# Kernel tuning notes

Measured on AMD Instinct MI355X. Metric: run time of the kernel, lower is better.

The kernel has to match this reference:

```python
import jax, jax.numpy as jnp
import numpy as np

HIDDEN = 4096
N_HEADS = 32
N_KV_HEADS = 8
HEAD_DIM = HIDDEN // N_HEADS
ROPE_BASE = 10000.0


def rotate_half(x):
    x1, x2 = jnp.split(x, 2, axis=-1)
    return jnp.concatenate((-x2, x1), axis=-1)


def rope_cos_sin(seq_len, dtype=jnp.float32):
    inv_freq = 1.0 / (ROPE_BASE ** (jnp.arange(0, HEAD_DIM, 2, dtype=jnp.float32) / HEAD_DIM))
    t = jnp.arange(seq_len, dtype=jnp.float32)
    freqs = jnp.einsum('i,j->ij', t, inv_freq)          # [S, D/2]
    emb = jnp.concatenate((freqs, freqs), axis=-1)       # [S, D]
    return jnp.cos(emb).astype(dtype), jnp.sin(emb).astype(dtype)


def setup_inputs() -> dict:
    key = jax.random.key(0)
    ks = jax.random.split(key, 6)
    bsz, q_len = 2, 2048
    hidden_states = jax.random.normal(ks[0], (bsz, q_len, HIDDEN), dtype=jnp.float32)
    # causal additive mask [bsz, 1, q, kv]
    neg = jnp.finfo(jnp.float32).min
    causal = jnp.where(jnp.tril(jnp.ones((q_len, q_len), dtype=bool)), 0.0, neg)
    attention_mask = jnp.broadcast_to(causal, (bsz, 1, q_len, q_len)).astype(jnp.float32)
    position_ids = jnp.broadcast_to(jnp.arange(q_len, dtype=jnp.int64), (bsz, q_len))
    s = 1.0 / np.sqrt(HIDDEN)
    Wq = jax.random.normal(ks[1], (HIDDEN, N_HEADS * HEAD_DIM), dtype=jnp.float32) * s
    Wk = jax.random.normal(ks[2], (HIDDEN, N_KV_HEADS * HEAD_DIM), dtype=jnp.float32) * s
    Wv = jax.random.normal(ks[3], (HIDDEN, N_KV_HEADS * HEAD_DIM), dtype=jnp.float32) * s
    Wo = jax.random.normal(ks[4], (N_HEADS * HEAD_DIM, HIDDEN), dtype=jnp.float32) * s
    return {"hidden_states": hidden_states, "attention_mask": attention_mask,
            "position_ids": position_ids, "Wq": Wq, "Wk": Wk, "Wv": Wv, "Wo": Wo}


def reference(hidden_states, attention_mask, position_ids, Wq, Wk, Wv, Wo):
    bsz, q_len, _ = hidden_states.shape
    groups = N_HEADS // N_KV_HEADS
    q = (hidden_states @ Wq).reshape(bsz, q_len, N_HEADS, HEAD_DIM).transpose(0, 2, 1, 3)
    k = (hidden_states @ Wk).reshape(bsz, q_len, N_KV_HEADS, HEAD_DIM).transpose(0, 2, 1, 3)
    v = (hidden_states @ Wv).reshape(bsz, q_len, N_KV_HEADS, HEAD_DIM).transpose(0, 2, 1, 3)
    cos, sin = rope_cos_sin(q_len, hidden_states.dtype)
    cos = cos[position_ids][:, None]  # [B,1,S,D]
    sin = sin[position_ids][:, None]
    q = q * cos + rotate_half(q) * sin
    k = k * cos + rotate_half(k) * sin
    # GQA: repeat_interleave KV heads
    k = jnp.repeat(k, groups, axis=1)
    v = jnp.repeat(v, groups, axis=1)
    scores = jnp.einsum('bhqd,bhkd->bhqk', q, k) / np.sqrt(HEAD_DIM)
    scores = scores + attention_mask
    attn = jax.nn.softmax(scores.astype(jnp.float32), axis=-1).astype(q.dtype)
    out = jnp.einsum('bhqk,bhkd->bhqd', attn, v)
    out = out.transpose(0, 2, 1, 3).reshape(bsz, q_len, HIDDEN)
    return out @ Wo
```

## Files before the change

kernel.cpp:

```cpp
#include <hip/hip_runtime.h>
#include <cstdint>
#include <type_traits>

typedef unsigned short u16;
typedef __attribute__((ext_vector_type(8))) short bf16x8;
typedef __attribute__((ext_vector_type(4))) float f32x4;

__device__ __forceinline__ u16 f2bf(float f) {
  unsigned u = __float_as_uint(f);
  u += 0x7fffu + ((u >> 16) & 1u);
  return (u16)(u >> 16);
}
__device__ __forceinline__ float bf2f(u16 h) {
  return __uint_as_float(((unsigned)h) << 16);
}
__device__ __forceinline__ unsigned cvtpk(float lo, float hi) {
  unsigned r;
  asm("v_cvt_pk_bf16_f32 %0, %1, %2" : "=v"(r) : "v"(lo), "v"(hi));
  return r;
}

__device__ __forceinline__ void glds16(const u16* g, u16* l) {
  __builtin_amdgcn_global_load_lds((const __attribute__((address_space(1))) void*)g,
                                   (__attribute__((address_space(3))) void*)l,
                                   16, 0, 0);
}

#define MFMA16(a, b, c) __builtin_amdgcn_mfma_f32_16x16x32_bf16((a), (b), (c), 0, 0, 0)

__global__ __launch_bounds__(256) void k_f32_to_bf16(const float* __restrict__ in,
                                                     u16* __restrict__ out, int n4) {
  int i = blockIdx.x * 256 + threadIdx.x;
  if (i < n4) {
    float4 v = ((const float4*)in)[i];
    ushort4 o;
    o.x = f2bf(v.x); o.y = f2bf(v.y); o.z = f2bf(v.z); o.w = f2bf(v.w);
    ((ushort4*)out)[i] = o;
  }
}

__global__ __launch_bounds__(256) void k_transpose_f32_bf16(const float* __restrict__ in,
                                                            u16* __restrict__ out,
                                                            int R, int C) {
  __shared__ float t[32][33];
  int tx = threadIdx.x & 31, ty = threadIdx.x >> 5;
  int c0 = blockIdx.x * 32, r0 = blockIdx.y * 32;
#pragma unroll
  for (int i = 0; i < 4; ++i)
    t[ty + 8 * i][tx] = in[(size_t)(r0 + ty + 8 * i) * C + c0 + tx];
  __syncthreads();
#pragma unroll
  for (int i = 0; i < 4; ++i)
    out[(size_t)(c0 + ty + 8 * i) * R + r0 + tx] = f2bf(t[tx][ty + 8 * i]);
}

template <typename OutT>
__global__ __launch_bounds__(512, 2) void k_gemm256(const u16* __restrict__ A,
                                                    const u16* __restrict__ B,
                                                    OutT* __restrict__ C,
                                                    int M, int N, int K) {
  __shared__ __align__(16) u16 lds[65536];
  const int tid = threadIdx.x, wave = tid >> 6, lane = tid & 63;
  const int quad = lane >> 4, l15 = lane & 15, l7 = l15 & 7;
  const int wr = wave >> 2, wc = wave & 3;

  const int nwg = gridDim.x * gridDim.y;
  const int bid = blockIdx.y * gridDim.x + blockIdx.x;
  const int swz = (bid & 7) * (nwg >> 3) + (bid >> 3);
  const int m0 = (swz / gridDim.x) * 256, n0 = (swz % gridDim.x) * 256;

  const int lrow = lane >> 3, lx = (lane & 7) ^ lrow;
  const size_t rowK = (size_t)K;
  const u16* Abase = A + (size_t)(m0 + wr * 128 + (wave & 3) * 8 + lrow) * rowK + lx * 8;
  const u16* Bbase = B + (size_t)(n0 + wave * 16 + lrow) * rowK + lx * 8;

  u16* const AT0 = lds;
  u16* const BT0 = lds + 16384;
  u16* const AT1 = lds + 32768;
  u16* const BT1 = lds + 49152;
  const int adst = (wr * 128 + (wave & 3) * 8) * 64;
  const int bdst = wave * 16 * 64;

#define STAGE_A(DST, la, kk) \
  glds16(Abase + (size_t)((la) * 32) * rowK + (kk), (DST) + adst + (la) * 2048)
#define STAGE_B(DST, g, kk)                                                      \
  glds16(Bbase + (size_t)((((g) >> 1) * 128 + ((g) & 1) * 8)) * rowK + (kk),     \
         (DST) + bdst + (((g) >> 1) * 128 + ((g) & 1) * 8) * 64)

  const int aoff = (wr * 128 + l15) * 64;
  const int boff = (wc * 64 + l15) * 64;
  const int ck0 = (quad ^ l7) * 8;
  const int ck1 = ((quad + 4) ^ l7) * 8;

  STAGE_B(BT0, 0, 0); STAGE_B(BT0, 1, 0); STAGE_B(BT0, 2, 0); STAGE_B(BT0, 3, 0);
  STAGE_A(AT0, 0, 0); STAGE_A(AT0, 1, 0); STAGE_A(AT0, 2, 0); STAGE_A(AT0, 3, 0);
  f32x4 acc[8][4] = {};
  asm volatile("s_waitcnt vmcnt(3)\ns_barrier" ::: "memory");

#define GPHASE(MP, STG1, STG2, VN)                                              \
  {                                                                             \
    bf16x8 a00 = *(const bf16x8*)&AT[aoff + (2 * (MP)) * 1024 + ck0];           \
    bf16x8 a01 = *(const bf16x8*)&AT[aoff + (2 * (MP)) * 1024 + ck1];           \
    bf16x8 a10 = *(const bf16x8*)&AT[aoff + (2 * (MP) + 1) * 1024 + ck0];       \
    bf16x8 a11 = *(const bf16x8*)&AT[aoff + (2 * (MP) + 1) * 1024 + ck1];       \
    STG1;                                                                       \
    STG2;                                                                       \
    asm volatile("s_barrier" ::: "memory");                                     \
    asm volatile("s_waitcnt lgkmcnt(0)" ::: "memory");                          \
    __builtin_amdgcn_sched_barrier(0);                                          \
    __builtin_amdgcn_s_setprio(1);                                              \
    _Pragma("unroll")                                                           \
    for (int nf = 0; nf < 4; ++nf) {                                            \
      acc[2 * (MP)][nf] = MFMA16(a00, bq[nf][0], acc[2 * (MP)][nf]);            \
      acc[2 * (MP)][nf] = MFMA16(a01, bq[nf][1], acc[2 * (MP)][nf]);            \
      acc[2 * (MP) + 1][nf] = MFMA16(a10, bq[nf][0], acc[2 * (MP) + 1][nf]);    \
      acc[2 * (MP) + 1][nf] = MFMA16(a11, bq[nf][1], acc[2 * (MP) + 1][nf]);    \
    }                                                                           \
    __builtin_amdgcn_s_setprio(0);                                              \
    asm volatile("s_waitcnt vmcnt(" #VN ")\ns_barrier" ::: "memory");           \
  }

  const int nt = K >> 6;
  for (int kt = 0; kt < nt; ++kt) {
    u16* const AT = (kt & 1) ? AT1 : AT0;
    u16* const BT = (kt & 1) ? BT1 : BT0;
    u16* const ATn = (kt & 1) ? AT0 : AT1;
    u16* const BTn = (kt & 1) ? BT0 : BT1;
    const int kk = (kt + 1 < nt) ? ((kt + 1) << 6) : 0;

    bf16x8 bq[4][2];
    {
      bf16x8 a00 = *(const bf16x8*)&AT[aoff + 0 * 1024 + ck0];
      bf16x8 a01 = *(const bf16x8*)&AT[aoff + 0 * 1024 + ck1];
      bf16x8 a10 = *(const bf16x8*)&AT[aoff + 1 * 1024 + ck0];
      bf16x8 a11 = *(const bf16x8*)&AT[aoff + 1 * 1024 + ck1];
#pragma unroll
      for (int nf = 0; nf < 4; ++nf) {
        bq[nf][0] = *(const bf16x8*)&BT[boff + nf * 1024 + ck0];
        bq[nf][1] = *(const bf16x8*)&BT[boff + nf * 1024 + ck1];
      }
      STAGE_B(BTn, 0, kk);
      STAGE_B(BTn, 1, kk);
      asm volatile("s_barrier" ::: "memory");
      asm volatile("s_waitcnt lgkmcnt(0)" ::: "memory");
      __builtin_amdgcn_sched_barrier(0);
      __builtin_amdgcn_s_setprio(1);
#pragma unroll
      for (int nf = 0; nf < 4; ++nf) {
        acc[0][nf] = MFMA16(a00, bq[nf][0], acc[0][nf]);
        acc[0][nf] = MFMA16(a01, bq[nf][1], acc[0][nf]);
        acc[1][nf] = MFMA16(a10, bq[nf][0], acc[1][nf]);
        acc[1][nf] = MFMA16(a11, bq[nf][1], acc[1][nf]);
      }
      __builtin_amdgcn_s_setprio(0);
      asm volatile("s_waitcnt vmcnt(4)\ns_barrier" ::: "memory");
    }
    GPHASE(1, STAGE_B(BTn, 2, kk), STAGE_B(BTn, 3, kk), 5)
    GPHASE(2, STAGE_A(ATn, 0, kk), STAGE_A(ATn, 1, kk), 6)
    GPHASE(3, STAGE_A(ATn, 2, kk), STAGE_A(ATn, 3, kk), 3)
  }
#undef GPHASE
#undef STAGE_A
#undef STAGE_B

  asm volatile("s_waitcnt vmcnt(0)" ::: "memory");

#pragma unroll
  for (int mf = 0; mf < 8; ++mf)
#pragma unroll
    for (int nf = 0; nf < 4; ++nf) {
      const int row = m0 + wr * 128 + mf * 16 + quad * 4;
      const int col = n0 + wc * 64 + nf * 16 + l15;
#pragma unroll
      for (int r = 0; r < 4; ++r) {
        float v = acc[mf][nf][r];
        if constexpr (std::is_same<OutT, u16>::value)
          C[(size_t)(row + r) * N + col] = f2bf(v);
        else
          C[(size_t)(row + r) * N + col] = v;
      }
    }
}

__global__ __launch_bounds__(256) void k_rope(u16* __restrict__ qkv) {
  int row = blockIdx.x;
  int s = row & 2047;
  u16* base = qkv + (size_t)row * 6144;
  for (int p = threadIdx.x; p < 2560; p += 256) {
    int d, col;
    if (p < 2048) { d = p & 63; col = (p >> 6) * 128 + d; }
    else { int pk = p - 2048; d = pk & 63; col = 4096 + (pk >> 6) * 128 + d; }
    float f = exp2f((float)d * (-13.287712379549449f / 64.0f));
    float th = (float)s * f;
    float c = cosf(th), sn = sinf(th);
    float x1 = bf2f(base[col]), x2 = bf2f(base[col + 64]);
    base[col]      = f2bf(x1 * c - x2 * sn);
    base[col + 64] = f2bf(x2 * c + x1 * sn);
  }
}

__global__ __launch_bounds__(256) void k_vt(const u16* __restrict__ qkv, u16* __restrict__ vt) {
  __shared__ u16 t[32][33];
  int tx = threadIdx.x & 31, ty = threadIdx.x >> 5;
  int s0 = blockIdx.x * 32, d0 = blockIdx.y * 32, g = blockIdx.z;
  int b = g >> 3, kvh = g & 7;
  const u16* in = qkv + (size_t)(b * 2048) * 6144 + 5120 + kvh * 128;
  u16* out = vt + (size_t)g * 128 * 2048;
#pragma unroll
  for (int i = 0; i < 4; ++i)
    t[ty + 8 * i][tx] = in[(size_t)(s0 + ty + 8 * i) * 6144 + d0 + tx];
  __syncthreads();
#pragma unroll
  for (int i = 0; i < 4; ++i)
    out[(size_t)(d0 + ty + 8 * i) * 2048 + s0 + tx] = t[tx][ty + 8 * i];
}

__global__ __launch_bounds__(256) void k_flash(const u16* __restrict__ qkv,
                                               const u16* __restrict__ vt,
                                               u16* __restrict__ ao) {
  __shared__ __align__(16) u16 Ks[64][128];
  __shared__ __align__(16) u16 Vs[128][64];
  __shared__ __align__(16) u16 Ps[4][16][64];
  const int tid = threadIdx.x, wave = tid >> 6, lane = tid & 63;
  const int quad = lane >> 4, l15 = lane & 15, l7 = l15 & 7;
  const int bh = blockIdx.x, b = bh >> 5, h = bh & 31, kvh = h >> 2;
  const int q0 = (31 - (int)blockIdx.y) * 64;

  bf16x8 aq[4];
  {
    const u16* qp = qkv + (size_t)(b * 2048 + q0 + wave * 16 + l15) * 6144 + h * 128 + quad * 8;
#pragma unroll
    for (int c = 0; c < 4; ++c) aq[c] = *(const bf16x8*)(qp + c * 32);
  }

  f32x4 oacc[8] = {};
  float m_r = -1e30f, l_r = 0.f;

  const u16* kbase = qkv + (size_t)(b * 2048) * 6144 + 4096 + kvh * 128;
  const u16* vbase = vt + (size_t)(b * 8 + kvh) * 128 * 2048;

  const int krow = wave * 4 + (lane >> 4);
  const int kch = (lane & 15) ^ (krow & 7);
  const u16* ksrc0 = kbase + (size_t)krow * 6144 + kch * 8;
  const int vrow = wave * 8 + (lane >> 3);
  const int vch = (lane & 7) ^ (vrow & 7);
  const u16* vsrc0 = vbase + (size_t)vrow * 2048 + vch * 8;
  u16* KsW = &Ks[0][0] + wave * 512;
  u16* VsW = &Vs[0][0] + wave * 512;

  const float SC = 0.12751744f;
  const int qg = q0 + wave * 16 + l15;
  const int nk = q0 / 64 + 1;

  for (int kt = 0; kt < nk; ++kt) {
    const int k0 = kt * 64;
    __syncthreads();
#pragma unroll
    for (int it = 0; it < 4; ++it)
      glds16(ksrc0 + (size_t)(k0 + it * 16) * 6144, KsW + it * 2048);
#pragma unroll
    for (int it = 0; it < 4; ++it)
      glds16(vsrc0 + k0 + it * 65536, VsW + it * 2048);
    __syncthreads();

    f32x4 sacc[4] = {};
    __builtin_amdgcn_s_setprio(1);
#pragma unroll
    for (int c = 0; c < 4; ++c)
#pragma unroll
      for (int nt = 0; nt < 4; ++nt) {
        const bf16x8 bk = *(const bf16x8*)&Ks[nt * 16 + l15][((4 * c + quad) ^ l7) * 8];
        sacc[nt] = __builtin_amdgcn_mfma_f32_16x16x32_bf16(bk, aq[c], sacc[nt], 0, 0, 0);
      }
    __builtin_amdgcn_s_setprio(0);

    float p[16];
    if (kt == nk - 1) {
#pragma unroll
      for (int nt = 0; nt < 4; ++nt)
#pragma unroll
        for (int r = 0; r < 4; ++r) {
          const float v = sacc[nt][r] * SC;
          p[nt * 4 + r] = (k0 + nt * 16 + quad * 4 + r > qg) ? -3e38f : v;
        }
    } else {
#pragma unroll
      for (int nt = 0; nt < 4; ++nt)
#pragma unroll
        for (int r = 0; r < 4; ++r) p[nt * 4 + r] = sacc[nt][r] * SC;
    }

    float rm = p[0];
#pragma unroll
    for (int i = 1; i < 16; ++i) rm = fmaxf(rm, p[i]);
    rm = fmaxf(rm, __shfl_xor(rm, 16, 64));
    rm = fmaxf(rm, __shfl_xor(rm, 32, 64));

    if (__any(rm > m_r + 8.0f)) {
      const float mn = fmaxf(m_r, rm);
      const float alpha = exp2f(m_r - mn);
      m_r = mn;
      l_r *= alpha;
#pragma unroll
      for (int r = 0; r < 4; ++r) {
        const float ar = __shfl(alpha, quad * 4 + r, 64);
#pragma unroll
        for (int o = 0; o < 8; ++o) oacc[o][r] *= ar;
      }
    }

    float rs = 0.f;
#pragma unroll
    for (int i = 0; i < 16; ++i) { p[i] = exp2f(p[i] - m_r); rs += p[i]; }
    rs += __shfl_xor(rs, 16, 64);
    rs += __shfl_xor(rs, 32, 64);
    l_r += rs;

    char* psrow = (char*)&Ps[wave][0][0] + l15 * 128;
#pragma unroll
    for (int nt = 0; nt < 4; ++nt)
#pragma unroll
      for (int pr = 0; pr < 2; ++pr) {
        const unsigned pk = cvtpk(p[nt * 4 + pr * 2], p[nt * 4 + pr * 2 + 1]);
        const int csw = (2 * nt + (quad >> 1)) ^ l7;
        *(unsigned*)(psrow + csw * 16 + (quad & 1) * 8 + pr * 4) = pk;
      }

    __builtin_amdgcn_s_setprio(1);
#pragma unroll
    for (int kc = 0; kc < 2; ++kc) {
      const int cs = (4 * kc + quad) ^ l7;
      const bf16x8 ap = *(const bf16x8*)(psrow + cs * 16);
#pragma unroll
      for (int o = 0; o < 8; ++o) {
        const bf16x8 bv = *(const bf16x8*)&Vs[o * 16 + l15][cs * 8];
        oacc[o] = __builtin_amdgcn_mfma_f32_16x16x32_bf16(ap, bv, oacc[o], 0, 0, 0);
      }
    }
    __builtin_amdgcn_s_setprio(0);
  }

  const float inv = 1.0f / l_r;
  u16* op = ao + (size_t)(b * 2048 + q0 + wave * 16 + quad * 4) * 4096 + h * 128 + l15;
#pragma unroll
  for (int r = 0; r < 4; ++r) {
    const float ir = __shfl(inv, quad * 4 + r, 64);
#pragma unroll
    for (int o = 0; o < 8; ++o)
      op[(size_t)r * 4096 + o * 16] = f2bf(oacc[o][r] * ir);
  }
}

extern "C" void kernel_launch(void* const* d_in, const int* in_sizes, int n_in,
                              void* d_out, int out_size, void* d_ws, size_t ws_size,
                              hipStream_t stream) {
  const float* X  = (const float*)d_in[0];
  const float* Wq = (const float*)d_in[3];
  const float* Wk = (const float*)d_in[4];
  const float* Wv = (const float*)d_in[5];
  const float* Wo = (const float*)d_in[6];
  float* out = (float*)d_out;

  char* ws = (char*)d_ws;
  u16* Xb     = (u16*)(ws);
  u16* WqkvT  = (u16*)(ws + 33554432ull);
  u16* WoT    = (u16*)(ws + 83886080ull);
  u16* QKV    = (u16*)(ws + 117440512ull);
  u16* Vt     = (u16*)(ws + 167772160ull);
  u16* AO     = (u16*)(ws + 176160768ull);

  k_f32_to_bf16<<<16384, 256, 0, stream>>>(X, Xb, 4194304);
  k_transpose_f32_bf16<<<dim3(128, 128), 256, 0, stream>>>(Wq, WqkvT, 4096, 4096);
  k_transpose_f32_bf16<<<dim3(32, 128), 256, 0, stream>>>(Wk, WqkvT + (size_t)4096 * 4096, 4096, 1024);
  k_transpose_f32_bf16<<<dim3(32, 128), 256, 0, stream>>>(Wv, WqkvT + (size_t)5120 * 4096, 4096, 1024);
  k_transpose_f32_bf16<<<dim3(128, 128), 256, 0, stream>>>(Wo, WoT, 4096, 4096);
  k_gemm256<u16><<<dim3(24, 16), 512, 0, stream>>>(Xb, WqkvT, QKV, 4096, 6144, 4096);
  k_rope<<<4096, 256, 0, stream>>>(QKV);
  k_vt<<<dim3(64, 4, 16), 256, 0, stream>>>(QKV, Vt);
  k_flash<<<dim3(64, 32), 256, 0, stream>>>(QKV, Vt, AO);
  k_gemm256<float><<<dim3(16, 16), 512, 0, stream>>>(AO, WoT, out, 4096, 4096, 4096);
}
```

Measured before the change: 748.1 us.

## Replace phased interleaved GEMM pipeline with simple double-buffered prefetch loop

Replaces the four-phase K-loop, which interleaved global-to-LDS stage issues with MFMA groups under per-phase barriers, setprio and fine-grained vmcnt waits, with a simpler schedule. The new loop issues all next-tile loads up front, runs all MFMAs for the current tile, then does one full vmcnt(0) wait and a barrier per iteration. It also skips the dummy prefetch on the last iteration. This cuts barrier count and scheduling constraints, but gives up the fine interleaving and priority hints, and LDS reads are no longer explicitly fenced with lgkmcnt or sched barriers.

```diff
diff --git a/kernel.cpp b/kernel.cpp
--- a/kernel.cpp
+++ b/kernel.cpp
@@ -95,30 +95,8 @@
   STAGE_B(BT0, 0, 0); STAGE_B(BT0, 1, 0); STAGE_B(BT0, 2, 0); STAGE_B(BT0, 3, 0);
   STAGE_A(AT0, 0, 0); STAGE_A(AT0, 1, 0); STAGE_A(AT0, 2, 0); STAGE_A(AT0, 3, 0);
   f32x4 acc[8][4] = {};
-  asm volatile("s_waitcnt vmcnt(3)\ns_barrier" ::: "memory");
-
-#define GPHASE(MP, STG1, STG2, VN)                                              \
-  {                                                                             \
-    bf16x8 a00 = *(const bf16x8*)&AT[aoff + (2 * (MP)) * 1024 + ck0];           \
-    bf16x8 a01 = *(const bf16x8*)&AT[aoff + (2 * (MP)) * 1024 + ck1];           \
-    bf16x8 a10 = *(const bf16x8*)&AT[aoff + (2 * (MP) + 1) * 1024 + ck0];       \
-    bf16x8 a11 = *(const bf16x8*)&AT[aoff + (2 * (MP) + 1) * 1024 + ck1];       \
-    STG1;                                                                       \
-    STG2;                                                                       \
-    asm volatile("s_barrier" ::: "memory");                                     \
-    asm volatile("s_waitcnt lgkmcnt(0)" ::: "memory");                          \
-    __builtin_amdgcn_sched_barrier(0);                                          \
-    __builtin_amdgcn_s_setprio(1);                                              \
-    _Pragma("unroll")                                                           \
-    for (int nf = 0; nf < 4; ++nf) {                                            \
-      acc[2 * (MP)][nf] = MFMA16(a00, bq[nf][0], acc[2 * (MP)][nf]);            \
-      acc[2 * (MP)][nf] = MFMA16(a01, bq[nf][1], acc[2 * (MP)][nf]);            \
-      acc[2 * (MP) + 1][nf] = MFMA16(a10, bq[nf][0], acc[2 * (MP) + 1][nf]);    \
-      acc[2 * (MP) + 1][nf] = MFMA16(a11, bq[nf][1], acc[2 * (MP) + 1][nf]);    \
-    }                                                                           \
-    __builtin_amdgcn_s_setprio(0);                                              \
-    asm volatile("s_waitcnt vmcnt(" #VN ")\ns_barrier" ::: "memory");           \
-  }
+  asm volatile("s_waitcnt vmcnt(0)" ::: "memory");
+  asm volatile("s_barrier" ::: "memory");
 
   const int nt = K >> 6;
   for (int kt = 0; kt < nt; ++kt) {
@@ -126,44 +104,41 @@
     u16* const BT = (kt & 1) ? BT1 : BT0;
     u16* const ATn = (kt & 1) ? AT0 : AT1;
     u16* const BTn = (kt & 1) ? BT0 : BT1;
-    const int kk = (kt + 1 < nt) ? ((kt + 1) << 6) : 0;
+
+    if (kt + 1 < nt) {
+      const int kk = (kt + 1) << 6;
+      STAGE_B(BTn, 0, kk); STAGE_B(BTn, 1, kk);
+      STAGE_B(BTn, 2, kk); STAGE_B(BTn, 3, kk);
+      STAGE_A(ATn, 0, kk); STAGE_A(ATn, 1, kk);
+      STAGE_A(ATn, 2, kk); STAGE_A(ATn, 3, kk);
+    }
 
     bf16x8 bq[4][2];
-    {
-      bf16x8 a00 = *(const bf16x8*)&AT[aoff + 0 * 1024 + ck0];
-      bf16x8 a01 = *(const bf16x8*)&AT[aoff + 0 * 1024 + ck1];
-      bf16x8 a10 = *(const bf16x8*)&AT[aoff + 1 * 1024 + ck0];
-      bf16x8 a11 = *(const bf16x8*)&AT[aoff + 1 * 1024 + ck1];
+#pragma unroll
+    for (int nf = 0; nf < 4; ++nf) {
+      bq[nf][0] = *(const bf16x8*)&BT[boff + nf * 1024 + ck0];
+      bq[nf][1] = *(const bf16x8*)&BT[boff + nf * 1024 + ck1];
+    }
+#pragma unroll
+    for (int mp = 0; mp < 4; ++mp) {
+      bf16x8 a00 = *(const bf16x8*)&AT[aoff + (2 * mp) * 1024 + ck0];
+      bf16x8 a01 = *(const bf16x8*)&AT[aoff + (2 * mp) * 1024 + ck1];
+      bf16x8 a10 = *(const bf16x8*)&AT[aoff + (2 * mp + 1) * 1024 + ck0];
+      bf16x8 a11 = *(const bf16x8*)&AT[aoff + (2 * mp + 1) * 1024 + ck1];
 #pragma unroll
       for (int nf = 0; nf < 4; ++nf) {
-        bq[nf][0] = *(const bf16x8*)&BT[boff + nf * 1024 + ck0];
-        bq[nf][1] = *(const bf16x8*)&BT[boff + nf * 1024 + ck1];
-      }
-      STAGE_B(BTn, 0, kk);
-      STAGE_B(BTn, 1, kk);
-      asm volatile("s_barrier" ::: "memory");
-      asm volatile("s_waitcnt lgkmcnt(0)" ::: "memory");
-      __builtin_amdgcn_sched_barrier(0);
-      __builtin_amdgcn_s_setprio(1);
-#pragma unroll
-      for (int nf = 0; nf < 4; ++nf) {
-        acc[0][nf] = MFMA16(a00, bq[nf][0], acc[0][nf]);
-        acc[0][nf] = MFMA16(a01, bq[nf][1], acc[0][nf]);
-        acc[1][nf] = MFMA16(a10, bq[nf][0], acc[1][nf]);
-        acc[1][nf] = MFMA16(a11, bq[nf][1], acc[1][nf]);
-      }
-      __builtin_amdgcn_s_setprio(0);
-      asm volatile("s_waitcnt vmcnt(4)\ns_barrier" ::: "memory");
-    }
-    GPHASE(1, STAGE_B(BTn, 2, kk), STAGE_B(BTn, 3, kk), 5)
-    GPHASE(2, STAGE_A(ATn, 0, kk), STAGE_A(ATn, 1, kk), 6)
-    GPHASE(3, STAGE_A(ATn, 2, kk), STAGE_A(ATn, 3, kk), 3)
-  }
-#undef GPHASE
+        acc[2 * mp][nf] = MFMA16(a00, bq[nf][0], acc[2 * mp][nf]);
+        acc[2 * mp][nf] = MFMA16(a01, bq[nf][1], acc[2 * mp][nf]);
+        acc[2 * mp + 1][nf] = MFMA16(a10, bq[nf][0], acc[2 * mp + 1][nf]);
+        acc[2 * mp + 1][nf] = MFMA16(a11, bq[nf][1], acc[2 * mp + 1][nf]);
+      }
+    }
+
+    asm volatile("s_waitcnt vmcnt(0)" ::: "memory");
+    asm volatile("s_barrier" ::: "memory");
+  }
 #undef STAGE_A
 #undef STAGE_B
-
-  asm volatile("s_waitcnt vmcnt(0)" ::: "memory");
 
 #pragma unroll
   for (int mf = 0; mf < 8; ++mf)
```

Result: faster. 715.9 us (-4.3%).
